# Kernel tuning notes

Hardware: AMD Instinct MI355X
Metric: run time of the kernel (lower is better)

## Reference

```python
import jax, jax.numpy as jnp
import numpy as np

DIMS, KS, NPOS = 128, 3, 8
B, H, W, NK = 4, 240, 320, 4000


def setup_inputs() -> dict:
    key = jax.random.key(0)
    ks = jax.random.split(key, 8)
    x = jax.random.normal(ks[0], (B, DIMS, H, W), jnp.float32)
    # keypoints normalized to [-1,1] (module maps them to pixel coords)
    keypoints = jax.random.uniform(ks[1], (B, NK, 2), jnp.float32, minval=-0.95, maxval=0.95)
    w1 = jax.random.normal(ks[2], (2 * NPOS, DIMS, KS, KS), jnp.float32) * 0.05
    b1 = jax.random.normal(ks[3], (2 * NPOS,), jnp.float32) * 0.05
    w2 = jax.random.normal(ks[4], (2 * NPOS, 2 * NPOS), jnp.float32) * 0.2
    b2 = jax.random.normal(ks[5], (2 * NPOS,), jnp.float32) * 0.05
    sf_w = jax.random.normal(ks[6], (DIMS, DIMS), jnp.float32) * 0.05
    agg_w = jax.random.uniform(ks[7], (NPOS, DIMS, DIMS), jnp.float32)  # torch.rand init
    return dict(x=x, keypoints=keypoints, w1=w1, b1=b1, w2=w2, b2=b2, sf_w=sf_w, agg_w=agg_w)


def _get_patches(xi, cx, cy, ps):
    # xi: [c,h,w]; cx,cy: [N] int top-left corners -> patches [N,c,ps,ps]
    off = jnp.arange(ps)
    iy = cy[:, None, None] + off[None, :, None]  # [N,ps,1]
    ix = cx[:, None, None] + off[None, None, :]  # [N,1,ps]
    return xi[:, iy, ix].transpose(1, 0, 2, 3)


def _bilinear_zeros(xi, px, py):
    # grid_sample bilinear, padding_mode='zeros', align_corners=True; px,py pixel coords [M]
    c, h, w = xi.shape
    x0 = jnp.floor(px)
    y0 = jnp.floor(py)
    wx = px - x0
    wy = py - y0

    def gat(xc, yc):
        valid = (xc >= 0) & (xc <= w - 1) & (yc >= 0) & (yc <= h - 1)
        xi_c = jnp.clip(xc, 0, w - 1).astype(jnp.int32)
        yi_c = jnp.clip(yc, 0, h - 1).astype(jnp.int32)
        return xi[:, yi_c, xi_c] * valid.astype(xi.dtype)  # [c,M]

    return (gat(x0, y0) * (1 - wx) * (1 - wy)
            + gat(x0 + 1, y0) * wx * (1 - wy)
            + gat(x0, y0 + 1) * (1 - wx) * wy
            + gat(x0 + 1, y0 + 1) * wx * wy)


def _sddh_one(xi, kpts, w1, b1, w2, b2, sf_w, agg_w):
    c, h, w = xi.shape
    wh = jnp.array([w - 1, h - 1], jnp.float32)
    max_off = max(h, w) / 4.0
    kw = (kpts / 2.0 + 0.5) * wh                       # [N,2] pixel coords (x,y)
    kwl = kw.astype(jnp.int32)                          # .long() trunc (coords >=0 -> floor)
    corner = (kwl.astype(jnp.float32) - KS / 2 + 1).astype(jnp.int32)
    cx = jnp.clip(corner[:, 0], 0, w - 1 - KS)
    cy = jnp.clip(corner[:, 1], 0, h - 1 - KS)
    patch = _get_patches(xi, cx, cy, KS)                # [N,c,ks,ks]
    # offset_conv: 3x3 valid conv on 3x3 patch == full contraction, then ReLU, then 1x1 conv
    o = jnp.einsum('ncij,ocij->no', patch, w1) + b1
    o = jax.nn.relu(o)
    o = o @ w2.T + b2                                   # [N, 2*NPOS]
    o = jnp.clip(o, -max_off, max_off)
    offset = o.reshape(-1, 2, NPOS).transpose(0, 2, 1)  # [N,NPOS,2] (x,y)
    pos = kw[:, None, :] + offset                       # sample positions in pixels
    # (the module normalizes to [-1,1] then grid_sample(align_corners=True) unnormalizes back)
    feats = _bilinear_zeros(xi, pos[..., 0].reshape(-1), pos[..., 1].reshape(-1))
    feats = feats.reshape(c, -1, NPOS).transpose(1, 0, 2)  # [N,c,NPOS]
    feats = jax.nn.selu(jnp.einsum('dc,ncp->ndp', sf_w, feats))  # sf_conv 1x1 + selu
    descs = jnp.einsum('ncp,pcd->nd', feats, agg_w)
    norm = jnp.linalg.norm(descs, axis=1, keepdims=True)
    return descs / jnp.maximum(norm, 1e-12)             # F.normalize p=2 dim=1


def reference(x, keypoints, w1, b1, w2, b2, sf_w, agg_w):
    return jax.vmap(_sddh_one, in_axes=(0, 0, None, None, None, None, None, None))(
        x, keypoints, w1, b1, w2, b2, sf_w, agg_w)  # [B,NK,DIMS]
```

## Files before the change

kernel.cpp:

```cpp
#include <hip/hip_runtime.h>
#include <cstdint>
#include <cmath>

#define BB   4
#define NK   4000
#define NKP  (BB*NK)
#define CH   128
#define HH   240
#define WW   320
#define HWSZ (HH*WW)
#define NPOS 8

typedef __attribute__((ext_vector_type(8))) short short8;
typedef __attribute__((ext_vector_type(8))) unsigned short ushort8;
typedef __attribute__((ext_vector_type(4))) float f32x4;

static constexpr size_t OFF_POS  = 32768000;
static constexpr size_t OFF_SFT  = 65536000;
static constexpr size_t OFF_W1T  = 65601536;
static constexpr size_t OFF_XCL  = 65675264;
static constexpr size_t OFF_SFB  = 222961664;
static constexpr size_t OFF_AGB  = 222994432;
static constexpr size_t WS_FULL  = 223256576;
static constexpr size_t WS_MIN   = 65675264;

__device__ __forceinline__ unsigned short f2bf(float f) {
    unsigned int u = __float_as_uint(f);
    u += 0x7fff + ((u >> 16) & 1);
    return (unsigned short)(u >> 16);
}
__device__ __forceinline__ float bf2f(unsigned short u) {
    return __uint_as_float((unsigned)u << 16);
}

__global__ __launch_bounds__(256) void k_prep(const float* __restrict__ sfw,
                                              const float* __restrict__ w1,
                                              const float* __restrict__ aggw,
                                              float* __restrict__ sfT,
                                              float* __restrict__ w1T,
                                              unsigned short* __restrict__ sfB,
                                              unsigned short* __restrict__ agB)
{
    int id = blockIdx.x * 256 + threadIdx.x;
    if (id < 16384) {
        int cc = id >> 7, dd = id & 127;
        sfT[cc * 128 + dd] = sfw[dd * 128 + cc];
    } else if (id < 16384 + 18432) {
        int j = id - 16384;
        int o = j / 1152, r = j % 1152;
        int k = r >> 7, c = r & 127;
        w1T[j] = w1[o * 1152 + c * 9 + k];
    } else if (id < 16384 + 18432 + 16384) {
        int idx = id - (16384 + 18432);
        int j = idx & 7, lane = (idx >> 3) & 63, nt = (idx >> 9) & 7, kc32 = (idx >> 12) & 3;
        int k = kc32 * 32 + (lane >> 4) * 8 + j;
        int n = nt * 16 + (lane & 15);
        sfB[idx] = f2bf(sfw[n * 128 + k]);
    } else if (id < 16384 + 18432 + 16384 + 131072) {
        int idx = id - (16384 + 18432 + 16384);
        int local = idx & 16383, kc = idx >> 14;
        int j = local & 7, lane = (local >> 3) & 63, nt = (local >> 9) & 7, kc32 = (local >> 12) & 3;
        int k = kc * 128 + kc32 * 32 + (lane >> 4) * 8 + j;
        int n = nt * 16 + (lane & 15);
        agB[idx] = f2bf(aggw[(size_t)k * 128 + n]);
    }
}

__global__ __launch_bounds__(256) void k_tr(const float* __restrict__ x,
                                            unsigned short* __restrict__ xclb)
{
    const int b  = blockIdx.y;
    const int p0 = blockIdx.x * 64;
    const int t  = threadIdx.x;
    __shared__ float tile[64 * 129];

    #pragma unroll
    for (int i = 0; i < 8; ++i) {
        int flat = i * 256 + t;
        int c  = flat >> 4;
        int p4 = flat & 15;
        float4 v = *(const float4*)(x + ((size_t)(b * 128 + c)) * HWSZ + p0 + p4 * 4);
        tile[(p4 * 4 + 0) * 129 + c] = v.x;
        tile[(p4 * 4 + 1) * 129 + c] = v.y;
        tile[(p4 * 4 + 2) * 129 + c] = v.z;
        tile[(p4 * 4 + 3) * 129 + c] = v.w;
    }
    __syncthreads();
    #pragma unroll
    for (int j = 0; j < 4; ++j) {
        int flat = j * 256 + t;
        int p  = flat >> 4;
        int c8 = flat & 15;
        ushort8 o;
        #pragma unroll
        for (int k = 0; k < 8; ++k)
            o[k] = f2bf(tile[p * 129 + c8 * 8 + k]);
        *(ushort8*)(xclb + ((size_t)b * HWSZ + p0 + p) * CH + c8 * 8) = o;
    }
}

__global__ __launch_bounds__(256) void k_mega(
    const unsigned short* __restrict__ xclb, const float* __restrict__ kp,
    const float* __restrict__ w1T, const float* __restrict__ b1,
    const float* __restrict__ w2,  const float* __restrict__ b2,
    const unsigned short* __restrict__ sfB,
    const unsigned short* __restrict__ agB,
    float* __restrict__ out)
{
    const int t  = threadIdx.x;
    const int n0 = blockIdx.x * 16;
    const int bi = n0 / NK;

    __shared__ __align__(16) char U[49664];
    float* wl = (float*)U;
    float* pl = (float*)(U + 24832);
    char*  AsB = U;
    char*  GlB = U + 16384;
    float* Dl = (float*)U;
    __shared__ float  o1l[16 * 16];
    __shared__ float  kwl[16 * 2];
    __shared__ float2 posl[128];

    if (t < 16) {
        const int n = n0 + t;
        float kx = kp[2 * n], ky = kp[2 * n + 1];
        kwl[t * 2 + 0] = (kx * 0.5f + 0.5f) * (float)(WW - 1);
        kwl[t * 2 + 1] = (ky * 0.5f + 0.5f) * (float)(HH - 1);
    }

    const int o_c  = t >> 4;
    const int kp_c = t & 15;
    float acc0 = 0.f, acc1 = 0.f;

    for (int h = 0; h < 3; ++h) {
        if (h) __syncthreads();
        #pragma unroll
        for (int i = 0; i < 6; ++i) {
            int idx = i * 256 + t;
            int o = idx / 96, c4 = idx % 96;
            *(float4*)&wl[o * 388 + c4 * 4] =
                *(const float4*)&w1T[o * 1152 + h * 384 + c4 * 4];
        }
        #pragma unroll
        for (int i = 0; i < 3; ++i) {
            int idx = i * 256 + t;
            int kk = idx / 48, r = idx % 48;
            int px = r >> 4, c8 = r & 15;
            int n = n0 + kk;
            float kx = kp[2 * n], ky = kp[2 * n + 1];
            float kwx = (kx * 0.5f + 0.5f) * (float)(WW - 1);
            float kwy = (ky * 0.5f + 0.5f) * (float)(HH - 1);
            int cx = (int)((float)((int)kwx) - 0.5f);
            int cy = (int)((float)((int)kwy) - 0.5f);
            cx = min(max(cx, 0), WW - 4);
            cy = min(max(cy, 0), HH - 4);
            const unsigned short* xb = xclb + (size_t)bi * HWSZ * CH;
            ushort8 raw = *(const ushort8*)(xb + ((size_t)(cy + h) * WW + (cx + px)) * CH + c8 * 8);
            float* dst = &pl[kk * 388 + px * 128 + c8 * 8];
            #pragma unroll
            for (int k = 0; k < 8; ++k) dst[k] = bf2f(raw[k]);
        }
        __syncthreads();
        #pragma unroll 4
        for (int q = 0; q < 96; q += 2) {
            float4 w0 = *(const float4*)&wl[o_c * 388 + q * 4];
            float4 p0 = *(const float4*)&pl[kp_c * 388 + q * 4];
            float4 w1v = *(const float4*)&wl[o_c * 388 + q * 4 + 4];
            float4 p1 = *(const float4*)&pl[kp_c * 388 + q * 4 + 4];
            acc0 = fmaf(w0.x, p0.x, fmaf(w0.y, p0.y, fmaf(w0.z, p0.z, fmaf(w0.w, p0.w, acc0))));
            acc1 = fmaf(w1v.x, p1.x, fmaf(w1v.y, p1.y, fmaf(w1v.z, p1.z, fmaf(w1v.w, p1.w, acc1))));
        }
    }

    __syncthreads();
    o1l[kp_c * 16 + o_c] = fmaxf(acc0 + acc1 + b1[o_c], 0.f);
    __syncthreads();

    if (t < 128) {
        const int kk = t >> 3, j = t & 7;
        float sx = b2[j], sy = b2[8 + j];
        #pragma unroll
        for (int i = 0; i < 16; ++i) {
            float v = o1l[kk * 16 + i];
            sx = fmaf(v, w2[j * 16 + i], sx);
            sy = fmaf(v, w2[(8 + j) * 16 + i], sy);
        }
        sx = fminf(fmaxf(sx, -80.f), 80.f);
        sy = fminf(fmaxf(sy, -80.f), 80.f);
        posl[kk * 8 + j] = make_float2(kwl[kk * 2 + 0] + sx, kwl[kk * 2 + 1] + sy);
    }
    __syncthreads();

    const int w = t >> 6, l = t & 63;
    const int fr = l & 15, fq = l >> 4;
    const int grp = t >> 5, lane32 = t & 31;
    const unsigned short* xb = xclb + (size_t)bi * HWSZ * CH;

    for (int chunk = 0; chunk < 2; ++chunk) {
        if (chunk) __syncthreads();
        #pragma unroll
        for (int it = 0; it < 8; ++it) {
            const int r = it * 8 + grp;
            float2 P = posl[chunk * 64 + r];
            const float x0 = floorf(P.x), y0 = floorf(P.y);
            const float wx = P.x - x0, wy = P.y - y0;
            float4 acc = {0.f, 0.f, 0.f, 0.f};
            #pragma unroll
            for (int dy = 0; dy < 2; ++dy) {
                const float yc = y0 + (float)dy;
                const bool vy = (yc >= 0.f) && (yc <= (float)(HH - 1));
                const int  yi = (int)fminf(fmaxf(yc, 0.f), (float)(HH - 1));
                const float wyv = dy ? wy : (1.f - wy);
                #pragma unroll
                for (int dx = 0; dx < 2; ++dx) {
                    const float xc = x0 + (float)dx;
                    const bool vx = (xc >= 0.f) && (xc <= (float)(WW - 1));
                    const int  xi = (int)fminf(fmaxf(xc, 0.f), (float)(WW - 1));
                    const float wgt = (vx && vy) ? (dx ? wx : (1.f - wx)) * wyv : 0.f;
                    ushort4 rv = *(const ushort4*)(xb + ((size_t)yi * WW + xi) * CH + lane32 * 4);
                    acc.x = fmaf(bf2f(rv.x), wgt, acc.x);
                    acc.y = fmaf(bf2f(rv.y), wgt, acc.y);
                    acc.z = fmaf(bf2f(rv.z), wgt, acc.z);
                    acc.w = fmaf(bf2f(rv.w), wgt, acc.w);
                }
            }
            ushort4 o = {f2bf(acc.x), f2bf(acc.y), f2bf(acc.z), f2bf(acc.w)};
            unsigned byte = (unsigned)(r * 256 + lane32 * 8);
            byte ^= ((unsigned)(r & 7)) << 4;
            *(ushort4*)(AsB + byte) = o;
        }
        __syncthreads();

        short8 a[4];
        #pragma unroll
        for (int q = 0; q < 4; ++q) {
            const int row = w * 16 + fr;
            unsigned byte = (unsigned)(row * 256 + q * 64 + fq * 16);
            byte ^= ((unsigned)(row & 7)) << 4;
            a[q] = *(const short8*)(AsB + byte);
        }

        f32x4 acc[8];
        #pragma unroll
        for (int nt = 0; nt < 8; ++nt)
            #pragma unroll
            for (int r = 0; r < 4; ++r) acc[nt][r] = 0.f;

        #pragma unroll 2
        for (int nt = 0; nt < 8; ++nt) {
            short8 b[4];
            #pragma unroll
            for (int q = 0; q < 4; ++q)
                b[q] = *(const short8*)(sfB + ((size_t)(q * 8 + nt) * 64 + l) * 8);
            #pragma unroll
            for (int q = 0; q < 4; ++q)
                acc[nt] = __builtin_amdgcn_mfma_f32_16x16x32_bf16(a[q], b[q], acc[nt], 0, 0, 0);
        }

        #pragma unroll
        for (int nt = 0; nt < 8; ++nt)
            #pragma unroll
            for (int r = 0; r < 4; ++r) {
                float v = acc[nt][r];
                float e = v > 0.f ? v : 1.6732632423543772f * (__expf(v) - 1.f);
                const int row = chunk * 64 + w * 16 + fq * 4 + r;
                unsigned byte = (unsigned)(row * 256 + (nt * 16 + fr) * 2);
                byte ^= ((unsigned)((row >> 3) & 7)) << 4;
                *(unsigned short*)(GlB + byte) = f2bf(1.0507009873554805f * e);
            }
    }
    __syncthreads();

    f32x4 acc2[2];
    #pragma unroll
    for (int i = 0; i < 2; ++i)
        #pragma unroll
        for (int r = 0; r < 4; ++r) acc2[i][r] = 0.f;

    const int nt0 = w * 2;
    #pragma unroll 4
    for (int kk = 0; kk < 32; ++kk) {
        const int row = fr * 8 + (kk >> 2);
        unsigned byte = (unsigned)(row * 256 + ((kk & 3) * 32 + fq * 8) * 2);
        byte ^= ((unsigned)((row >> 3) & 7)) << 4;
        short8 a2 = *(const short8*)(GlB + byte);
        #pragma unroll
        for (int i = 0; i < 2; ++i) {
            short8 b2 = *(const short8*)(agB + (size_t)(kk >> 2) * 16384 +
                ((size_t)(((kk & 3) * 8 + nt0 + i) * 64 + l)) * 8);
            acc2[i] = __builtin_amdgcn_mfma_f32_16x16x32_bf16(a2, b2, acc2[i], 0, 0, 0);
        }
    }

    #pragma unroll
    for (int i = 0; i < 2; ++i)
        #pragma unroll
        for (int r = 0; r < 4; ++r)
            Dl[(fq * 4 + r) * 132 + w * 32 + i * 16 + fr] = acc2[i][r];
    __syncthreads();

    {
        const int row = t >> 4, seg = t & 15;
        const float* dr = Dl + row * 132 + seg * 8;
        float4 d0 = *(const float4*)(dr);
        float4 d1 = *(const float4*)(dr + 4);
        float s = d0.x*d0.x + d0.y*d0.y + d0.z*d0.z + d0.w*d0.w
                + d1.x*d1.x + d1.y*d1.y + d1.z*d1.z + d1.w*d1.w;
        #pragma unroll
        for (int m = 1; m < 16; m <<= 1) s += __shfl_xor(s, m);
        const float inv = 1.f / fmaxf(sqrtf(s), 1e-12f);
        float* op = out + (size_t)(n0 + row) * 128 + seg * 8;
        float4 o0 = {d0.x*inv, d0.y*inv, d0.z*inv, d0.w*inv};
        float4 o1 = {d1.x*inv, d1.y*inv, d1.z*inv, d1.w*inv};
        *(float4*)(op)     = o0;
        *(float4*)(op + 4) = o1;
    }
}

__global__ __launch_bounds__(128) void k_sample(
    const float* __restrict__ x,  const float* __restrict__ kp,
    const float* __restrict__ w1, const float* __restrict__ b1,
    const float* __restrict__ w2, const float* __restrict__ b2,
    float* __restrict__ feats)
{
    const int n  = blockIdx.x;
    const int bi = n / NK;
    const int t  = threadIdx.x;

    __shared__ __align__(16) float patch[CH * 9];
    __shared__ float red[16 * 8];
    __shared__ float o1[16];
    __shared__ float offv[16];

    const float kx  = kp[(size_t)n * 2 + 0];
    const float ky  = kp[(size_t)n * 2 + 1];
    const float kwx = (kx * 0.5f + 0.5f) * (float)(WW - 1);
    const float kwy = (ky * 0.5f + 0.5f) * (float)(HH - 1);
    const int kwlx = (int)kwx;
    const int kwly = (int)kwy;
    int cx = (int)((float)kwlx - 0.5f);
    int cy = (int)((float)kwly - 0.5f);
    cx = min(max(cx, 0), WW - 1 - 3);
    cy = min(max(cy, 0), HH - 1 - 3);

    const float* xb = x + ((size_t)bi * CH + t) * HWSZ;
    {
        const float* p0 = xb + cy * WW + cx;
        #pragma unroll
        for (int i = 0; i < 3; ++i) {
            patch[t * 9 + i * 3 + 0] = p0[i * WW + 0];
            patch[t * 9 + i * 3 + 1] = p0[i * WW + 1];
            patch[t * 9 + i * 3 + 2] = p0[i * WW + 2];
        }
    }
    __syncthreads();
    {
        const int o = t & 15, g = t >> 4;
        const float4* wp = (const float4*)(w1 + o * 1152 + g * 144);
        const float4* pp = (const float4*)(patch + g * 144);
        float s = 0.f;
        #pragma unroll
        for (int q = 0; q < 36; ++q) {
            float4 wv = wp[q];
            float4 pv = pp[q];
            s = fmaf(wv.x, pv.x, fmaf(wv.y, pv.y, fmaf(wv.z, pv.z, fmaf(wv.w, pv.w, s))));
        }
        red[o * 8 + g] = s;
    }
    __syncthreads();
    if (t < 16) {
        float s = b1[t];
        #pragma unroll
        for (int g = 0; g < 8; ++g) s += red[t * 8 + g];
        o1[t] = fmaxf(s, 0.f);
    }
    __syncthreads();
    if (t < 16) {
        float s = b2[t];
        #pragma unroll
        for (int j = 0; j < 16; ++j) s = fmaf(o1[j], w2[t * 16 + j], s);
        offv[t] = fminf(fmaxf(s, -80.f), 80.f);
    }
    __syncthreads();

    #pragma unroll
    for (int p = 0; p < NPOS; ++p) {
        const float px = kwx + offv[p];
        const float py = kwy + offv[8 + p];
        const float x0 = floorf(px), y0 = floorf(py);
        const float wx = px - x0, wy = py - y0;
        float acc = 0.f;
        #pragma unroll
        for (int dy = 0; dy < 2; ++dy) {
            const float yc = y0 + (float)dy;
            const bool vy = (yc >= 0.f) && (yc <= (float)(HH - 1));
            const int  yi = (int)fminf(fmaxf(yc, 0.f), (float)(HH - 1));
            const float wyv = dy ? wy : (1.f - wy);
            #pragma unroll
            for (int dx = 0; dx < 2; ++dx) {
                const float xc = x0 + (float)dx;
                const bool vx = (xc >= 0.f) && (xc <= (float)(WW - 1));
                const int  xi = (int)fminf(fmaxf(xc, 0.f), (float)(WW - 1));
                const float wxv = dx ? wx : (1.f - wx);
                float v = xb[yi * WW + xi];
                v = (vx && vy) ? v : 0.f;
                acc = fmaf(v, wxv * wyv, acc);
            }
        }
        feats[((size_t)n * 8 + p) * CH + t] = acc;
    }
}

__global__ __launch_bounds__(256) void k_sf_legacy(float* __restrict__ gbuf,
                                                   const float* __restrict__ sfT)
{
    const int m0 = blockIdx.x * 64;
    const int t  = threadIdx.x;
    __shared__ __align__(16) float AT[128 * 68];

    #pragma unroll
    for (int i = 0; i < 32; ++i) {
        int flat = i * 256 + t;
        int mm = flat >> 7, kk = flat & 127;
        AT[kk * 68 + mm] = gbuf[(size_t)(m0 + mm) * 128 + kk];
    }
    __syncthreads();

    const int tx = t & 31, ty = t >> 5;
    const int d0 = tx * 4, mb = ty * 8;
    float acc[8][4];
    #pragma unroll
    for (int i = 0; i < 8; ++i)
        #pragma unroll
        for (int j = 0; j < 4; ++j) acc[i][j] = 0.f;

    #pragma unroll 4
    for (int k = 0; k < 128; ++k) {
        float4 a0 = *(const float4*)(AT + k * 68 + mb);
        float4 a1 = *(const float4*)(AT + k * 68 + mb + 4);
        float4 bq = *(const float4*)(sfT + k * 128 + d0);
        float a[8] = {a0.x, a0.y, a0.z, a0.w, a1.x, a1.y, a1.z, a1.w};
        float b4[4] = {bq.x, bq.y, bq.z, bq.w};
        #pragma unroll
        for (int i = 0; i < 8; ++i)
            #pragma unroll
            for (int j = 0; j < 4; ++j)
                acc[i][j] = fmaf(a[i], b4[j], acc[i][j]);
    }

    #pragma unroll
    for (int i = 0; i < 8; ++i) {
        float4 o;
        float* ov = &o.x;
        #pragma unroll
        for (int j = 0; j < 4; ++j) {
            float v = acc[i][j];
            float r = v > 0.f ? v : 1.6732632423543772f * expm1f(v);
            ov[j] = 1.0507009873554805f * r;
        }
        *(float4*)(gbuf + (size_t)(m0 + mb + i) * 128 + d0) = o;
    }
}

__global__ __launch_bounds__(256) void k_agg_mono(const float* __restrict__ gbuf,
                                                  const float* __restrict__ aggw,
                                                  float* __restrict__ out)
{
    const int m0 = blockIdx.x * 64;
    const int t  = threadIdx.x;
    __shared__ __align__(16) float AT[128 * 68];

    const int tx = t & 31, ty = t >> 5;
    const int d0 = tx * 4, mb = ty * 8;
    float acc[8][4];
    #pragma unroll
    for (int i = 0; i < 8; ++i)
        #pragma unroll
        for (int j = 0; j < 4; ++j) acc[i][j] = 0.f;

    for (int kc = 0; kc < 8; ++kc) {
        __syncthreads();
        #pragma unroll
        for (int i = 0; i < 32; ++i) {
            int flat = i * 256 + t;
            int mm = flat >> 7, kk = flat & 127;
            AT[kk * 68 + mm] = gbuf[(size_t)(m0 + mm) * 1024 + kc * 128 + kk];
        }
        __syncthreads();
        #pragma unroll 4
        for (int kk = 0; kk < 128; ++kk) {
            float4 a0 = *(const float4*)(AT + kk * 68 + mb);
            float4 a1 = *(const float4*)(AT + kk * 68 + mb + 4);
            float4 bq = *(const float4*)(aggw + (size_t)(kc * 128 + kk) * 128 + d0);
            float a[8] = {a0.x, a0.y, a0.z, a0.w, a1.x, a1.y, a1.z, a1.w};
            float b4[4] = {bq.x, bq.y, bq.z, bq.w};
            #pragma unroll
            for (int i = 0; i < 8; ++i)
                #pragma unroll
                for (int j = 0; j < 4; ++j)
                    acc[i][j] = fmaf(a[i], b4[j], acc[i][j]);
        }
    }

    #pragma unroll
    for (int i = 0; i < 8; ++i) {
        float s = acc[i][0] * acc[i][0] + acc[i][1] * acc[i][1]
                + acc[i][2] * acc[i][2] + acc[i][3] * acc[i][3];
        #pragma unroll
        for (int m = 16; m; m >>= 1) s += __shfl_xor(s, m);
        const float inv = 1.f / fmaxf(sqrtf(s), 1e-12f);
        float4 o = {acc[i][0] * inv, acc[i][1] * inv, acc[i][2] * inv, acc[i][3] * inv};
        *(float4*)(out + (size_t)(m0 + mb + i) * 128 + d0) = o;
    }
}

extern "C" void kernel_launch(void* const* d_in, const int* in_sizes, int n_in,
                              void* d_out, int out_size, void* d_ws, size_t ws_size,
                              hipStream_t stream)
{
    const float* x   = (const float*)d_in[0];
    const float* kp  = (const float*)d_in[1];
    const float* w1  = (const float*)d_in[2];
    const float* b1  = (const float*)d_in[3];
    const float* w2  = (const float*)d_in[4];
    const float* b2  = (const float*)d_in[5];
    const float* sfw = (const float*)d_in[6];
    const float* agg = (const float*)d_in[7];
    float* out = (float*)d_out;

    if (ws_size < WS_MIN) return;

    char*  ws    = (char*)d_ws;
    float* sfT   = (float*)(ws + OFF_SFT);
    float* w1T   = (float*)(ws + OFF_W1T);
    unsigned short* xclb = (unsigned short*)(ws + OFF_XCL);
    unsigned short* sfB  = (unsigned short*)(ws + OFF_SFB);
    unsigned short* agB  = (unsigned short*)(ws + OFF_AGB);

    k_prep<<<712, 256, 0, stream>>>(sfw, w1, agg, sfT, w1T, sfB, agB);

    if (ws_size >= WS_FULL) {
        dim3 grid(HWSZ / 64, BB);
        k_tr  <<<grid, 256, 0, stream>>>(x, xclb);
        k_mega<<<NKP / 16, 256, 0, stream>>>(xclb, kp, w1T, b1, w2, b2, sfB, agB, out);
    } else {
        float* feats = (float*)ws;
        k_sample   <<<NKP, 128, 0, stream>>>(x, kp, w1, b1, w2, b2, feats);
        k_sf_legacy<<<2000, 256, 0, stream>>>(feats, sfT);
        k_agg_mono <<<250,  256, 0, stream>>>(feats, agg, out);
    }
}
```

Baseline: 320.3 us.

## Gather bilinear samples directly into MFMA registers, shrink LDS, raise occupancy

Each lane now computes the bilinear-sampled bf16 values for its own MFMA A-fragment rows straight from global memory, so the LDS staging tile and its barriers are gone. The offset-conv patch is stored in LDS as raw bf16 rather than fp32, and the per-keypoint corner coordinates are computed once into shared memory instead of per thread. Together these shrink the LDS allocation, and launch_bounds now asks for 4 blocks per CU. The tradeoff is more scattered per-lane 16-byte gathers and register pressure under the occupancy hint.

```diff
diff --git a/kernel.cpp b/kernel.cpp
--- a/kernel.cpp
+++ b/kernel.cpp
@@ -99,7 +99,7 @@
     }
 }
 
-__global__ __launch_bounds__(256) void k_mega(
+__global__ __launch_bounds__(256, 4) void k_mega(
     const unsigned short* __restrict__ xclb, const float* __restrict__ kp,
     const float* __restrict__ w1T, const float* __restrict__ b1,
     const float* __restrict__ w2,  const float* __restrict__ b2,
@@ -111,26 +111,35 @@
     const int n0 = blockIdx.x * 16;
     const int bi = n0 / NK;
 
-    __shared__ __align__(16) char U[49664];
+    __shared__ __align__(16) char U[37376];
     float* wl = (float*)U;
-    float* pl = (float*)(U + 24832);
-    char*  AsB = U;
-    char*  GlB = U + 16384;
+    unsigned short* plb = (unsigned short*)(U + 24832);
+    char*  GlB = U;
     float* Dl = (float*)U;
     __shared__ float  o1l[16 * 16];
     __shared__ float  kwl[16 * 2];
+    __shared__ int2   cxyl[16];
     __shared__ float2 posl[128];
 
     if (t < 16) {
         const int n = n0 + t;
         float kx = kp[2 * n], ky = kp[2 * n + 1];
-        kwl[t * 2 + 0] = (kx * 0.5f + 0.5f) * (float)(WW - 1);
-        kwl[t * 2 + 1] = (ky * 0.5f + 0.5f) * (float)(HH - 1);
-    }
+        float kwx = (kx * 0.5f + 0.5f) * (float)(WW - 1);
+        float kwy = (ky * 0.5f + 0.5f) * (float)(HH - 1);
+        kwl[t * 2 + 0] = kwx;
+        kwl[t * 2 + 1] = kwy;
+        int cx = (int)((float)((int)kwx) - 0.5f);
+        int cy = (int)((float)((int)kwy) - 0.5f);
+        cx = min(max(cx, 0), WW - 4);
+        cy = min(max(cy, 0), HH - 4);
+        cxyl[t] = make_int2(cx, cy);
+    }
+    __syncthreads();
 
     const int o_c  = t >> 4;
     const int kp_c = t & 15;
     float acc0 = 0.f, acc1 = 0.f;
+    const unsigned short* xb = xclb + (size_t)bi * HWSZ * CH;
 
     for (int h = 0; h < 3; ++h) {
         if (h) __syncthreads();
@@ -146,29 +155,20 @@
             int idx = i * 256 + t;
             int kk = idx / 48, r = idx % 48;
             int px = r >> 4, c8 = r & 15;
-            int n = n0 + kk;
-            float kx = kp[2 * n], ky = kp[2 * n + 1];
-            float kwx = (kx * 0.5f + 0.5f) * (float)(WW - 1);
-            float kwy = (ky * 0.5f + 0.5f) * (float)(HH - 1);
-            int cx = (int)((float)((int)kwx) - 0.5f);
-            int cy = (int)((float)((int)kwy) - 0.5f);
-            cx = min(max(cx, 0), WW - 4);
-            cy = min(max(cy, 0), HH - 4);
-            const unsigned short* xb = xclb + (size_t)bi * HWSZ * CH;
-            ushort8 raw = *(const ushort8*)(xb + ((size_t)(cy + h) * WW + (cx + px)) * CH + c8 * 8);
-            float* dst = &pl[kk * 388 + px * 128 + c8 * 8];
-            #pragma unroll
-            for (int k = 0; k < 8; ++k) dst[k] = bf2f(raw[k]);
+            int2 c = cxyl[kk];
+            ushort8 raw = *(const ushort8*)(xb + ((size_t)(c.y + h) * WW + (c.x + px)) * CH + c8 * 8);
+            *(ushort8*)&plb[kk * 392 + px * 128 + c8 * 8] = raw;
         }
         __syncthreads();
         #pragma unroll 4
-        for (int q = 0; q < 96; q += 2) {
-            float4 w0 = *(const float4*)&wl[o_c * 388 + q * 4];
-            float4 p0 = *(const float4*)&pl[kp_c * 388 + q * 4];
-            float4 w1v = *(const float4*)&wl[o_c * 388 + q * 4 + 4];
-            float4 p1 = *(const float4*)&pl[kp_c * 388 + q * 4 + 4];
-            acc0 = fmaf(w0.x, p0.x, fmaf(w0.y, p0.y, fmaf(w0.z, p0.z, fmaf(w0.w, p0.w, acc0))));
-            acc1 = fmaf(w1v.x, p1.x, fmaf(w1v.y, p1.y, fmaf(w1v.z, p1.z, fmaf(w1v.w, p1.w, acc1))));
+        for (int g = 0; g < 48; ++g) {
+            float4 w0  = *(const float4*)&wl[o_c * 388 + g * 8];
+            float4 w1v = *(const float4*)&wl[o_c * 388 + g * 8 + 4];
+            ushort8 p8 = *(const ushort8*)&plb[kp_c * 392 + g * 8];
+            acc0 = fmaf(w0.x, bf2f(p8[0]), fmaf(w0.y, bf2f(p8[1]),
+                   fmaf(w0.z, bf2f(p8[2]), fmaf(w0.w, bf2f(p8[3]), acc0))));
+            acc1 = fmaf(w1v.x, bf2f(p8[4]), fmaf(w1v.y, bf2f(p8[5]),
+                   fmaf(w1v.z, bf2f(p8[6]), fmaf(w1v.w, bf2f(p8[7]), acc1))));
         }
     }
 
@@ -193,51 +193,48 @@
 
     const int w = t >> 6, l = t & 63;
     const int fr = l & 15, fq = l >> 4;
-    const int grp = t >> 5, lane32 = t & 31;
-    const unsigned short* xb = xclb + (size_t)bi * HWSZ * CH;
 
     for (int chunk = 0; chunk < 2; ++chunk) {
-        if (chunk) __syncthreads();
-        #pragma unroll
-        for (int it = 0; it < 8; ++it) {
-            const int r = it * 8 + grp;
-            float2 P = posl[chunk * 64 + r];
-            const float x0 = floorf(P.x), y0 = floorf(P.y);
-            const float wx = P.x - x0, wy = P.y - y0;
-            float4 acc = {0.f, 0.f, 0.f, 0.f};
-            #pragma unroll
-            for (int dy = 0; dy < 2; ++dy) {
-                const float yc = y0 + (float)dy;
-                const bool vy = (yc >= 0.f) && (yc <= (float)(HH - 1));
-                const int  yi = (int)fminf(fmaxf(yc, 0.f), (float)(HH - 1));
-                const float wyv = dy ? wy : (1.f - wy);
-                #pragma unroll
-                for (int dx = 0; dx < 2; ++dx) {
-                    const float xc = x0 + (float)dx;
-                    const bool vx = (xc >= 0.f) && (xc <= (float)(WW - 1));
-                    const int  xi = (int)fminf(fmaxf(xc, 0.f), (float)(WW - 1));
-                    const float wgt = (vx && vy) ? (dx ? wx : (1.f - wx)) * wyv : 0.f;
-                    ushort4 rv = *(const ushort4*)(xb + ((size_t)yi * WW + xi) * CH + lane32 * 4);
-                    acc.x = fmaf(bf2f(rv.x), wgt, acc.x);
-                    acc.y = fmaf(bf2f(rv.y), wgt, acc.y);
-                    acc.z = fmaf(bf2f(rv.z), wgt, acc.z);
-                    acc.w = fmaf(bf2f(rv.w), wgt, acc.w);
-                }
+        const int arow = chunk * 64 + w * 16 + fr;
+        float2 P = posl[arow];
+        const float x0 = floorf(P.x), y0 = floorf(P.y);
+        const float wx = P.x - x0, wy = P.y - y0;
+        const unsigned short* cp[4];
+        float cw[4];
+        #pragma unroll
+        for (int dy = 0; dy < 2; ++dy) {
+            const float yc = y0 + (float)dy;
+            const bool vy = (yc >= 0.f) && (yc <= (float)(HH - 1));
+            const int  yi = (int)fminf(fmaxf(yc, 0.f), (float)(HH - 1));
+            const float wyv = dy ? wy : (1.f - wy);
+            #pragma unroll
+            for (int dx = 0; dx < 2; ++dx) {
+                const float xc = x0 + (float)dx;
+                const bool vx = (xc >= 0.f) && (xc <= (float)(WW - 1));
+                const int  xi = (int)fminf(fmaxf(xc, 0.f), (float)(WW - 1));
+                cp[dy * 2 + dx] = xb + ((size_t)yi * WW + xi) * CH;
+                cw[dy * 2 + dx] = (vx && vy) ? (dx ? wx : (1.f - wx)) * wyv : 0.f;
             }
-            ushort4 o = {f2bf(acc.x), f2bf(acc.y), f2bf(acc.z), f2bf(acc.w)};
-            unsigned byte = (unsigned)(r * 256 + lane32 * 8);
-            byte ^= ((unsigned)(r & 7)) << 4;
-            *(ushort4*)(AsB + byte) = o;
-        }
-        __syncthreads();
+        }
 
         short8 a[4];
         #pragma unroll
         for (int q = 0; q < 4; ++q) {
-            const int row = w * 16 + fr;
-            unsigned byte = (unsigned)(row * 256 + q * 64 + fq * 16);
-            byte ^= ((unsigned)(row & 7)) << 4;
-            a[q] = *(const short8*)(AsB + byte);
+            const int ch = q * 32 + fq * 8;
+            ushort8 c0 = *(const ushort8*)(cp[0] + ch);
+            ushort8 c1 = *(const ushort8*)(cp[1] + ch);
+            ushort8 c2 = *(const ushort8*)(cp[2] + ch);
+            ushort8 c3 = *(const ushort8*)(cp[3] + ch);
+            short8 av;
+            #pragma unroll
+            for (int j = 0; j < 8; ++j) {
+                float s = fmaf(bf2f(c0[j]), cw[0], 0.f);
+                s = fmaf(bf2f(c1[j]), cw[1], s);
+                s = fmaf(bf2f(c2[j]), cw[2], s);
+                s = fmaf(bf2f(c3[j]), cw[3], s);
+                av[j] = (short)f2bf(s);
+            }
+            a[q] = av;
         }
 
         f32x4 acc[8];
@@ -292,6 +289,7 @@
         }
     }
 
+    __syncthreads();
     #pragma unroll
     for (int i = 0; i < 2; ++i)
         #pragma unroll
```

After: 301.3 us. -5.9%, faster.
